# Performance work log

Hardware: AMD Instinct MI355X
Metric: run time of the kernel (lower is better)

## Reference

```python
import jax, jax.numpy as jnp
import numpy as np

N_NODES = 100000
N_EDGES = 1600000
D_FEAT = 64      # per-node embedding dim; nin = 2*D_FEAT = 128
N_OUT = 64
NSLOPE = 0.2


def setup_inputs() -> dict:
    key = jax.random.key(0)
    k0, k1, k2, k3, k4, k5 = jax.random.split(key, 6)
    nodes = jax.random.normal(k0, (N_NODES, D_FEAT), dtype=jnp.float32)
    src = jax.random.randint(k1, (N_EDGES,), 0, N_NODES, dtype=jnp.int32)
    dst = jax.random.randint(k2, (N_EDGES,), 0, N_NODES, dtype=jnp.int32)
    # Linear(nin=2*D_FEAT, nout=N_OUT) weight/bias and Linear(nout,1,bias=False)
    W_w = jax.random.normal(k3, (N_OUT, 2 * D_FEAT), dtype=jnp.float32) * (2 * D_FEAT) ** -0.5
    W_b = jax.random.normal(k4, (N_OUT,), dtype=jnp.float32) * 0.02
    a_w = jax.random.normal(k5, (N_OUT,), dtype=jnp.float32) * N_OUT ** -0.5
    return {"nodes": nodes, "src": src, "dst": dst, "W_w": W_w, "W_b": W_b, "a_w": a_w}


def reference(nodes, src, dst, W_w, W_b, a_w):
    # Per edge: score = a( LeakyReLU( W [h_src ; h_dst] + b ) )
    # Split W over the concat so we project each node once, then gather.
    d = nodes.shape[1]
    W1, W2 = W_w[:, :d], W_w[:, d:]          # [nout, d] each
    p1 = nodes @ W1.T                        # [N, nout]
    p2 = nodes @ W2.T                        # [N, nout]
    hw = p1[src] + p2[dst] + W_b             # [E, nout]  (== W(cat(hi,hj)))
    act = jnp.where(hw >= 0, hw, NSLOPE * hw)  # LeakyReLU
    scores = act @ a_w                       # [E]
    # Sparse softmax over dim=1 of the [N,N] score matrix == segment softmax
    # over edges grouped by the row (src) index, numerically stabilized.
    n = nodes.shape[0]
    m = jax.ops.segment_max(scores, src, num_segments=n)   # [N]
    e = jnp.exp(scores - m[src])                            # [E]
    s = jax.ops.segment_sum(e, src, num_segments=n)         # [N]
    attn = e / s[src]                                       # [E]
    return attn
```

## Files before the change

### kernel.cpp

```cpp
#include <hip/hip_runtime.h>

#define NSLOPE 0.2f

typedef __attribute__((ext_vector_type(8))) short short8;
typedef __attribute__((ext_vector_type(4))) float floatx4;

static __device__ inline unsigned short f2bf(float f) {
    unsigned u = __float_as_uint(f);
    unsigned r = u + 0x7FFFu + ((u >> 16) & 1u);
    return (unsigned short)(r >> 16);
}
static __device__ inline float bflo(unsigned u) { return __uint_as_float(u << 16); }
static __device__ inline float bfhi(unsigned u) { return __uint_as_float(u & 0xFFFF0000u); }

#define PNB 128
#define AST 72

__global__ __launch_bounds__(256) void proj_mfma_kernel(
    const float* __restrict__ nodes, const float* __restrict__ Ww,
    const float* __restrict__ Wb,
    unsigned short* __restrict__ P1, unsigned short* __restrict__ P2,
    float* __restrict__ ssum, int nNodes)
{
    __shared__ unsigned short aT[PNB * AST];
    __shared__ unsigned short wT[128 * AST];
    const int t = threadIdx.x;
    const int base = blockIdx.x * PNB;

    if (t < PNB) { int n = base + t; if (n < nNodes) ssum[n] = 0.f; }

    for (int f = t; f < PNB * 16; f += 256) {
        int n = f >> 4, dpos = (f & 15) * 4;
        float4 v = make_float4(0.f, 0.f, 0.f, 0.f);
        if (base + n < nNodes) v = *(const float4*)(nodes + (size_t)(base + n) * 64 + dpos);
        ushort4 o;
        o.x = f2bf(v.x); o.y = f2bf(v.y); o.z = f2bf(v.z); o.w = f2bf(v.w);
        *(ushort4*)&aT[n * AST + dpos] = o;
    }
    for (int i = t; i < 2048; i += 256) {
        float4 v = *(const float4*)(Ww + i * 4);
        int o = i >> 5;
        int c = (i * 4) & 127;
        int j, k;
        if (c < 64) { j = o;      k = c;      }
        else        { j = 64 + o; k = c - 64; }
        ushort4 w4;
        w4.x = f2bf(v.x); w4.y = f2bf(v.y); w4.z = f2bf(v.z); w4.w = f2bf(v.w);
        *(ushort4*)&wT[j * AST + k] = w4;
    }
    __syncthreads();

    const int w = t >> 6, lane = t & 63;
    const int lr = lane & 15;
    const int lk = (lane >> 4) * 8;

    floatx4 acc[2][8];
    #pragma unroll
    for (int rt = 0; rt < 2; rt++)
        #pragma unroll
        for (int ct = 0; ct < 8; ct++) acc[rt][ct] = (floatx4){0.f, 0.f, 0.f, 0.f};

    #pragma unroll
    for (int ks = 0; ks < 2; ks++) {
        int k0 = ks * 32 + lk;
        short8 a0 = *(const short8*)&aT[((w * 2 + 0) * 16 + lr) * AST + k0];
        short8 a1 = *(const short8*)&aT[((w * 2 + 1) * 16 + lr) * AST + k0];
        #pragma unroll
        for (int ct = 0; ct < 8; ct++) {
            short8 b = *(const short8*)&wT[(ct * 16 + lr) * AST + k0];
            acc[0][ct] = __builtin_amdgcn_mfma_f32_16x16x32_bf16(a0, b, acc[0][ct], 0, 0, 0);
            acc[1][ct] = __builtin_amdgcn_mfma_f32_16x16x32_bf16(a1, b, acc[1][ct], 0, 0, 0);
        }
    }

    #pragma unroll
    for (int ct = 0; ct < 8; ct++) {
        int j = ct * 16 + lr;
        float bias = (j < 64) ? Wb[j] : 0.f;
        #pragma unroll
        for (int rt = 0; rt < 2; rt++) {
            #pragma unroll
            for (int r = 0; r < 4; r++) {
                int nl = (w * 2 + rt) * 16 + (lane >> 4) * 4 + r;
                int n = base + nl;
                if (n < nNodes) {
                    unsigned short val = f2bf(acc[rt][ct][r] + bias);
                    if (j < 64) P1[(size_t)n * 64 + j]      = val;
                    else        P2[(size_t)n * 64 + j - 64] = val;
                }
            }
        }
    }
}

__global__ __launch_bounds__(256) void edge_score_kernel(
    const unsigned short* __restrict__ P1, const unsigned short* __restrict__ P2,
    const int* __restrict__ src, const int* __restrict__ dst,
    const float* __restrict__ a_w,
    float* __restrict__ evals, float* __restrict__ ssum, int nE)
{
    int tid = blockIdx.x * 256 + threadIdx.x;
    int g   = tid >> 3;
    int sub = tid & 7;
    int e0  = g << 2;
    if (e0 >= nE) return;
    const bool full = (e0 + 4 <= nE);

    int4 sv, dv;
    if (full) {
        sv = *(const int4*)(src + e0);
        dv = *(const int4*)(dst + e0);
    } else {
        int a[4], b[4];
        #pragma unroll
        for (int i = 0; i < 4; i++) {
            int e = (e0 + i < nE) ? e0 + i : nE - 1;
            a[i] = src[e]; b[i] = dst[e];
        }
        sv = make_int4(a[0], a[1], a[2], a[3]);
        dv = make_int4(b[0], b[1], b[2], b[3]);
    }
    int s[4] = {sv.x, sv.y, sv.z, sv.w};
    int d[4] = {dv.x, dv.y, dv.z, dv.w};

    uint4 r1[4], r2[4];
    #pragma unroll
    for (int i = 0; i < 4; i++) r1[i] = *(const uint4*)(P1 + (size_t)s[i] * 64 + sub * 8);
    #pragma unroll
    for (int i = 0; i < 4; i++) r2[i] = *(const uint4*)(P2 + (size_t)d[i] * 64 + sub * 8);

    float4 a0 = *(const float4*)(a_w + sub * 8);
    float4 a1 = *(const float4*)(a_w + sub * 8 + 4);

    float partial[4];
    #pragma unroll
    for (int i = 0; i < 4; i++) {
        float p = 0.f, h;
        h = bflo(r1[i].x) + bflo(r2[i].x); h = (h >= 0.f) ? h : NSLOPE * h; p = fmaf(h, a0.x, p);
        h = bfhi(r1[i].x) + bfhi(r2[i].x); h = (h >= 0.f) ? h : NSLOPE * h; p = fmaf(h, a0.y, p);
        h = bflo(r1[i].y) + bflo(r2[i].y); h = (h >= 0.f) ? h : NSLOPE * h; p = fmaf(h, a0.z, p);
        h = bfhi(r1[i].y) + bfhi(r2[i].y); h = (h >= 0.f) ? h : NSLOPE * h; p = fmaf(h, a0.w, p);
        h = bflo(r1[i].z) + bflo(r2[i].z); h = (h >= 0.f) ? h : NSLOPE * h; p = fmaf(h, a1.x, p);
        h = bfhi(r1[i].z) + bfhi(r2[i].z); h = (h >= 0.f) ? h : NSLOPE * h; p = fmaf(h, a1.y, p);
        h = bflo(r1[i].w) + bflo(r2[i].w); h = (h >= 0.f) ? h : NSLOPE * h; p = fmaf(h, a1.z, p);
        h = bfhi(r1[i].w) + bfhi(r2[i].w); h = (h >= 0.f) ? h : NSLOPE * h; p = fmaf(h, a1.w, p);
        partial[i] = p;
    }

    #pragma unroll
    for (int i = 0; i < 4; i++) {
        partial[i] += __shfl_xor(partial[i], 1);
        partial[i] += __shfl_xor(partial[i], 2);
        partial[i] += __shfl_xor(partial[i], 4);
    }

    if (sub == 0) {
        float ev[4];
        #pragma unroll
        for (int i = 0; i < 4; i++) ev[i] = __expf(partial[i]);
        if (full) {
            *(float4*)(evals + e0) = make_float4(ev[0], ev[1], ev[2], ev[3]);
            #pragma unroll
            for (int i = 0; i < 4; i++) atomicAdd(&ssum[s[i]], ev[i]);
        } else {
            for (int i = 0; i < 4 && e0 + i < nE; i++) {
                evals[e0 + i] = ev[i];
                atomicAdd(&ssum[s[i]], ev[i]);
            }
        }
    }
}

__global__ __launch_bounds__(256) void normalize_kernel(
    const int* __restrict__ src, const float* __restrict__ ssum,
    float* __restrict__ out, int nE)
{
    int i = blockIdx.x * 256 + threadIdx.x;
    int e4 = i * 4;
    if (e4 + 3 < nE) {
        float4 ev = *(const float4*)(out + e4);
        int4   sv = *(const int4*)(src + e4);
        float4 r;
        r.x = ev.x / ssum[sv.x];
        r.y = ev.y / ssum[sv.y];
        r.z = ev.z / ssum[sv.z];
        r.w = ev.w / ssum[sv.w];
        *(float4*)(out + e4) = r;
    } else {
        for (int e = e4; e < nE; ++e) out[e] = out[e] / ssum[src[e]];
    }
}

extern "C" void kernel_launch(void* const* d_in, const int* in_sizes, int n_in,
                              void* d_out, int out_size, void* d_ws, size_t ws_size,
                              hipStream_t stream) {
    (void)n_in; (void)out_size; (void)ws_size;
    const float* nodes = (const float*)d_in[0];
    const int*   src   = (const int*)d_in[1];
    const int*   dst   = (const int*)d_in[2];
    const float* Ww    = (const float*)d_in[3];
    const float* Wb    = (const float*)d_in[4];
    const float* a_w   = (const float*)d_in[5];
    float* out = (float*)d_out;

    const int nNodes = in_sizes[0] / 64;
    const int nE     = in_sizes[1];

    unsigned short* P1   = (unsigned short*)d_ws;
    unsigned short* P2   = P1 + (size_t)nNodes * 64;
    float*          ssum = (float*)(P2 + (size_t)nNodes * 64);

    int nblocks_proj = (nNodes + PNB - 1) / PNB;
    proj_mfma_kernel<<<nblocks_proj, 256, 0, stream>>>(nodes, Ww, Wb, P1, P2, ssum, nNodes);

    long long ngroups = ((long long)nE + 3) / 4;
    int nblocks_edge = (int)((ngroups * 8 + 255) / 256);
    edge_score_kernel<<<nblocks_edge, 256, 0, stream>>>(P1, P2, src, dst, a_w, out, ssum, nE);

    int nthreads_norm = (nE + 3) / 4;
    int nblocks_norm  = (nthreads_norm + 255) / 256;
    normalize_kernel<<<nblocks_norm, 256, 0, stream>>>(src, ssum, out, nE);
}
```

Before: 127.4 us.

## Build CSR by source per call and compute segment softmax per node

Replaces the edge-parallel scoring with float atomics plus a separate normalize pass. The new path builds a CSR grouping of edges by source node on every call: histogram, three-stage scan, then an atomic scatter of (dst, edge id) pairs. A wave per source node then scores its edges, reusing that node's P1 row, and reduces the exp-sum in registers before writing normalized outputs. This drops the float atomics and the ssum gather. In exchange it adds five extra launches, integer atomics in both hist and scatter, and extra traffic for csrPack and tempE. The final writes to out are scattered, and the edge loop runs waves only partly active because each node has about 16 edges.

Result: slower. 289.6 us (+127.3%).

```diff
diff --git a/kernel.cpp b/kernel.cpp
--- a/kernel.cpp
+++ b/kernel.cpp
@@ -20,14 +20,14 @@
     const float* __restrict__ nodes, const float* __restrict__ Ww,
     const float* __restrict__ Wb,
     unsigned short* __restrict__ P1, unsigned short* __restrict__ P2,
-    float* __restrict__ ssum, int nNodes)
+    int* __restrict__ counts, int nNodes)
 {
     __shared__ unsigned short aT[PNB * AST];
     __shared__ unsigned short wT[128 * AST];
     const int t = threadIdx.x;
     const int base = blockIdx.x * PNB;
 
-    if (t < PNB) { int n = base + t; if (n < nNodes) ssum[n] = 0.f; }
+    if (t < PNB) { int n = base + t; if (n < nNodes) counts[n] = 0; }
 
     for (int f = t; f < PNB * 16; f += 256) {
         int n = f >> 4, dpos = (f & 15) * 4;
@@ -93,101 +93,128 @@
     }
 }
 
-__global__ __launch_bounds__(256) void edge_score_kernel(
+__global__ __launch_bounds__(256) void hist_kernel(const int* __restrict__ src,
+                                                   int* __restrict__ counts, int nE) {
+    int e = blockIdx.x * 256 + threadIdx.x;
+    if (e < nE) atomicAdd(&counts[src[e]], 1);
+}
+
+__global__ __launch_bounds__(256) void scan1_kernel(const int* __restrict__ counts,
+                                                    int* __restrict__ offs,
+                                                    int* __restrict__ bsum, int nNodes) {
+    __shared__ int sd[256];
+    int t = threadIdx.x;
+    int i = blockIdx.x * 256 + t;
+    int v = (i < nNodes) ? counts[i] : 0;
+    sd[t] = v; __syncthreads();
+    #pragma unroll
+    for (int o = 1; o < 256; o <<= 1) {
+        int x = (t >= o) ? sd[t - o] : 0;
+        __syncthreads();
+        sd[t] += x;
+        __syncthreads();
+    }
+    if (i < nNodes) offs[i] = sd[t] - v;
+    if (t == 255) bsum[blockIdx.x] = sd[255];
+}
+
+__global__ __launch_bounds__(512) void scan2_kernel(const int* __restrict__ bsum,
+                                                    int* __restrict__ bpre, int nb) {
+    __shared__ int sd[512];
+    int t = threadIdx.x;
+    int v = (t < nb) ? bsum[t] : 0;
+    sd[t] = v; __syncthreads();
+    #pragma unroll
+    for (int o = 1; o < 512; o <<= 1) {
+        int x = (t >= o) ? sd[t - o] : 0;
+        __syncthreads();
+        sd[t] += x;
+        __syncthreads();
+    }
+    if (t < nb) bpre[t] = sd[t] - v;
+}
+
+__global__ __launch_bounds__(256) void scan3_kernel(int* __restrict__ offs,
+                                                    const int* __restrict__ bpre,
+                                                    int* __restrict__ cursor,
+                                                    int nNodes, int nE) {
+    int i = blockIdx.x * 256 + threadIdx.x;
+    if (i < nNodes) {
+        int v = offs[i] + bpre[i >> 8];
+        offs[i] = v;
+        cursor[i] = v;
+    }
+    if (i == 0) offs[nNodes] = nE;
+}
+
+__global__ __launch_bounds__(256) void scatter_kernel(const int* __restrict__ src,
+                                                      const int* __restrict__ dst,
+                                                      int* __restrict__ cursor,
+                                                      uint2* __restrict__ csrPack, int nE) {
+    int e = blockIdx.x * 256 + threadIdx.x;
+    if (e < nE) {
+        int s = src[e];
+        int p = atomicAdd(&cursor[s], 1);
+        csrPack[p] = make_uint2((unsigned)dst[e], (unsigned)e);
+    }
+}
+
+__global__ __launch_bounds__(256) void csr_edge_kernel(
     const unsigned short* __restrict__ P1, const unsigned short* __restrict__ P2,
-    const int* __restrict__ src, const int* __restrict__ dst,
+    const int* __restrict__ offs, const uint2* __restrict__ csrPack,
     const float* __restrict__ a_w,
-    float* __restrict__ evals, float* __restrict__ ssum, int nE)
+    float* __restrict__ tempE, float* __restrict__ out, int nNodes)
 {
-    int tid = blockIdx.x * 256 + threadIdx.x;
-    int g   = tid >> 3;
-    int sub = tid & 7;
-    int e0  = g << 2;
-    if (e0 >= nE) return;
-    const bool full = (e0 + 4 <= nE);
-
-    int4 sv, dv;
-    if (full) {
-        sv = *(const int4*)(src + e0);
-        dv = *(const int4*)(dst + e0);
-    } else {
-        int a[4], b[4];
-        #pragma unroll
-        for (int i = 0; i < 4; i++) {
-            int e = (e0 + i < nE) ? e0 + i : nE - 1;
-            a[i] = src[e]; b[i] = dst[e];
-        }
-        sv = make_int4(a[0], a[1], a[2], a[3]);
-        dv = make_int4(b[0], b[1], b[2], b[3]);
-    }
-    int s[4] = {sv.x, sv.y, sv.z, sv.w};
-    int d[4] = {dv.x, dv.y, dv.z, dv.w};
-
-    uint4 r1[4], r2[4];
-    #pragma unroll
-    for (int i = 0; i < 4; i++) r1[i] = *(const uint4*)(P1 + (size_t)s[i] * 64 + sub * 8);
-    #pragma unroll
-    for (int i = 0; i < 4; i++) r2[i] = *(const uint4*)(P2 + (size_t)d[i] * 64 + sub * 8);
-
+    const int t = threadIdx.x;
+    const int n = blockIdx.x * 4 + (t >> 6);
+    if (n >= nNodes) return;
+    const int lane = t & 63, sub = lane & 7, g = lane >> 3;
+
+    const int o0 = offs[n], o1 = offs[n + 1];
+    if (o0 == o1) return;
+
+    uint4 r1 = *(const uint4*)(P1 + (size_t)n * 64 + sub * 8);
     float4 a0 = *(const float4*)(a_w + sub * 8);
     float4 a1 = *(const float4*)(a_w + sub * 8 + 4);
 
-    float partial[4];
-    #pragma unroll
-    for (int i = 0; i < 4; i++) {
+    float segacc = 0.f;
+    for (int base = o0; base < o1; base += 8) {
+        int idx = base + g;
+        bool act = (idx < o1);
+        uint2 pk = csrPack[act ? idx : o0];
+        uint4 r2 = *(const uint4*)(P2 + (size_t)pk.x * 64 + sub * 8);
+
         float p = 0.f, h;
-        h = bflo(r1[i].x) + bflo(r2[i].x); h = (h >= 0.f) ? h : NSLOPE * h; p = fmaf(h, a0.x, p);
-        h = bfhi(r1[i].x) + bfhi(r2[i].x); h = (h >= 0.f) ? h : NSLOPE * h; p = fmaf(h, a0.y, p);
-        h = bflo(r1[i].y) + bflo(r2[i].y); h = (h >= 0.f) ? h : NSLOPE * h; p = fmaf(h, a0.z, p);
-        h = bfhi(r1[i].y) + bfhi(r2[i].y); h = (h >= 0.f) ? h : NSLOPE * h; p = fmaf(h, a0.w, p);
-        h = bflo(r1[i].z) + bflo(r2[i].z); h = (h >= 0.f) ? h : NSLOPE * h; p = fmaf(h, a1.x, p);
-        h = bfhi(r1[i].z) + bfhi(r2[i].z); h = (h >= 0.f) ? h : NSLOPE * h; p = fmaf(h, a1.y, p);
-        h = bflo(r1[i].w) + bflo(r2[i].w); h = (h >= 0.f) ? h : NSLOPE * h; p = fmaf(h, a1.z, p);
-        h = bfhi(r1[i].w) + bfhi(r2[i].w); h = (h >= 0.f) ? h : NSLOPE * h; p = fmaf(h, a1.w, p);
-        partial[i] = p;
-    }
-
-    #pragma unroll
-    for (int i = 0; i < 4; i++) {
-        partial[i] += __shfl_xor(partial[i], 1);
-        partial[i] += __shfl_xor(partial[i], 2);
-        partial[i] += __shfl_xor(partial[i], 4);
-    }
-
-    if (sub == 0) {
-        float ev[4];
-        #pragma unroll
-        for (int i = 0; i < 4; i++) ev[i] = __expf(partial[i]);
-        if (full) {
-            *(float4*)(evals + e0) = make_float4(ev[0], ev[1], ev[2], ev[3]);
-            #pragma unroll
-            for (int i = 0; i < 4; i++) atomicAdd(&ssum[s[i]], ev[i]);
-        } else {
-            for (int i = 0; i < 4 && e0 + i < nE; i++) {
-                evals[e0 + i] = ev[i];
-                atomicAdd(&ssum[s[i]], ev[i]);
-            }
+        h = bflo(r1.x) + bflo(r2.x); h = (h >= 0.f) ? h : NSLOPE * h; p = fmaf(h, a0.x, p);
+        h = bfhi(r1.x) + bfhi(r2.x); h = (h >= 0.f) ? h : NSLOPE * h; p = fmaf(h, a0.y, p);
+        h = bflo(r1.y) + bflo(r2.y); h = (h >= 0.f) ? h : NSLOPE * h; p = fmaf(h, a0.z, p);
+        h = bfhi(r1.y) + bfhi(r2.y); h = (h >= 0.f) ? h : NSLOPE * h; p = fmaf(h, a0.w, p);
+        h = bflo(r1.z) + bflo(r2.z); h = (h >= 0.f) ? h : NSLOPE * h; p = fmaf(h, a1.x, p);
+        h = bfhi(r1.z) + bfhi(r2.z); h = (h >= 0.f) ? h : NSLOPE * h; p = fmaf(h, a1.y, p);
+        h = bflo(r1.w) + bflo(r2.w); h = (h >= 0.f) ? h : NSLOPE * h; p = fmaf(h, a1.z, p);
+        h = bfhi(r1.w) + bfhi(r2.w); h = (h >= 0.f) ? h : NSLOPE * h; p = fmaf(h, a1.w, p);
+
+        p += __shfl_xor(p, 1);
+        p += __shfl_xor(p, 2);
+        p += __shfl_xor(p, 4);
+
+        float ev = __expf(p);
+        if (act && sub == 0) {
+            tempE[idx] = ev;
+            segacc += ev;
         }
     }
-}
-
-__global__ __launch_bounds__(256) void normalize_kernel(
-    const int* __restrict__ src, const float* __restrict__ ssum,
-    float* __restrict__ out, int nE)
-{
-    int i = blockIdx.x * 256 + threadIdx.x;
-    int e4 = i * 4;
-    if (e4 + 3 < nE) {
-        float4 ev = *(const float4*)(out + e4);
-        int4   sv = *(const int4*)(src + e4);
-        float4 r;
-        r.x = ev.x / ssum[sv.x];
-        r.y = ev.y / ssum[sv.y];
-        r.z = ev.z / ssum[sv.z];
-        r.w = ev.w / ssum[sv.w];
-        *(float4*)(out + e4) = r;
-    } else {
-        for (int e = e4; e < nE; ++e) out[e] = out[e] / ssum[src[e]];
+
+    segacc += __shfl_xor(segacc, 8);
+    segacc += __shfl_xor(segacc, 16);
+    segacc += __shfl_xor(segacc, 32);
+    float rs = 1.0f / __shfl(segacc, 0);
+
+    __threadfence_block();
+
+    for (int idx = o0 + lane; idx < o1; idx += 64) {
+        uint2 pk = csrPack[idx];
+        out[pk.y] = tempE[idx] * rs;
     }
 }
 
@@ -206,18 +233,28 @@
     const int nNodes = in_sizes[0] / 64;
     const int nE     = in_sizes[1];
 
-    unsigned short* P1   = (unsigned short*)d_ws;
-    unsigned short* P2   = P1 + (size_t)nNodes * 64;
-    float*          ssum = (float*)(P2 + (size_t)nNodes * 64);
+    unsigned short* P1     = (unsigned short*)d_ws;
+    unsigned short* P2     = P1 + (size_t)nNodes * 64;
+    int*            counts = (int*)(P2 + (size_t)nNodes * 64);
+    int*            offs   = counts + nNodes;
+    int*            cursor = offs + nNodes + 2;
+    int*            bsum   = cursor + nNodes;
+    int*            bpre   = bsum + 512;
+    uint2*          csrPack= (uint2*)(bpre + 512);
+    float*          tempE  = (float*)(csrPack + nE);
+
+    const int nb_scan = (nNodes + 255) / 256;
 
     int nblocks_proj = (nNodes + PNB - 1) / PNB;
-    proj_mfma_kernel<<<nblocks_proj, 256, 0, stream>>>(nodes, Ww, Wb, P1, P2, ssum, nNodes);
-
-    long long ngroups = ((long long)nE + 3) / 4;
-    int nblocks_edge = (int)((ngroups * 8 + 255) / 256);
-    edge_score_kernel<<<nblocks_edge, 256, 0, stream>>>(P1, P2, src, dst, a_w, out, ssum, nE);
-
-    int nthreads_norm = (nE + 3) / 4;
-    int nblocks_norm  = (nthreads_norm + 255) / 256;
-    normalize_kernel<<<nblocks_norm, 256, 0, stream>>>(src, ssum, out, nE);
-}
+    proj_mfma_kernel<<<nblocks_proj, 256, 0, stream>>>(nodes, Ww, Wb, P1, P2, counts, nNodes);
+
+    int nblocks_e = (nE + 255) / 256;
+    hist_kernel<<<nblocks_e, 256, 0, stream>>>(src, counts, nE);
+    scan1_kernel<<<nb_scan, 256, 0, stream>>>(counts, offs, bsum, nNodes);
+    scan2_kernel<<<1, 512, 0, stream>>>(bsum, bpre, nb_scan);
+    scan3_kernel<<<nb_scan, 256, 0, stream>>>(offs, bpre, cursor, nNodes, nE);
+    scatter_kernel<<<nblocks_e, 256, 0, stream>>>(src, dst, cursor, csrPack, nE);
+
+    int nblocks_edge = (nNodes + 3) / 4;
+    csr_edge_kernel<<<nblocks_edge, 256, 0, stream>>>(P1, P2, offs, csrPack, a_w, tempE, out, nNodes);
+}
```
